# Kernel optimization log

Measured on AMD Instinct MI355X. Metric: run time of the kernel, lower is better.

Reference implementation:

```python
import jax, jax.numpy as jnp
import numpy as np


def setup_inputs() -> dict:
    key = jax.random.key(0)
    k1, k2, k3 = jax.random.split(key, 3)
    B, N, D = 4, 256, 128
    s = jax.random.normal(k1, (B, N, D), dtype=jnp.float32)
    W1 = jax.random.normal(k2, (3 * D, 2 * D), dtype=jnp.float32) * 0.02
    b1 = jnp.zeros((2 * D,), dtype=jnp.float32)
    W2 = jax.random.normal(k3, (2 * D, 1), dtype=jnp.float32) * 0.02
    b2 = jnp.zeros((1,), dtype=jnp.float32)
    return {"s": s, "W1": W1, "b1": b1, "W2": W2, "b2": b2, "K": 8}


def reference(s, W1, b1, W2, b2, K):
    B, N, D = s.shape
    si = jnp.broadcast_to(s[:, :, None, :], (B, N, N, D))
    sj = jnp.broadcast_to(s[:, None, :, :], (B, N, N, D))
    pair = jnp.concatenate([si, sj, si * sj], axis=-1)  # [B,N,N,3D]
    h = jax.nn.relu(pair @ W1 + b1)                      # [B,N,N,2D]
    scores = (h @ W2 + b2)[..., 0]                       # [B,N,N]
    k = min(int(K), N)
    _, idx = jax.lax.top_k(scores, k)                    # [B,N,K]
    # scatter ones at topk indices (indices are distinct per row)
    gate = jnp.sum(jax.nn.one_hot(idx, N, dtype=jnp.float32), axis=-2)  # [B,N,N]
    w = gate / jnp.clip(jnp.sum(gate, axis=-1, keepdims=True), 1.0)
    ctx = jnp.einsum('bij,bjd->bid', w, s)               # [B,N,D]
    return ctx, gate, w
```

## Files before the change

### kernel.cpp

```cpp
#include <hip/hip_runtime.h>
#include <hip/hip_bf16.h>
#include <math.h>

#define B_ 4
#define N_ 256
#define D_ 128
#define H_ 256
#define K_ 8

typedef __attribute__((ext_vector_type(8))) short short8;
typedef __attribute__((ext_vector_type(4))) float f32x4;

__device__ __forceinline__ unsigned short f2bf(float x) {
    union { __hip_bfloat16 h; unsigned short s; } u;
    u.h = __float2bfloat16(x);
    return u.s;
}
__device__ __forceinline__ float bf2f(unsigned short b) {
    unsigned v = ((unsigned)b) << 16;
    return __builtin_bit_cast(float, v);
}
__device__ __forceinline__ unsigned pk2(float x, float y) {
    union { __hip_bfloat162 h; unsigned u; } c;
    c.h = __float22bfloat162_rn(float2{x, y});
    return c.u;
}
__device__ __forceinline__ void gld_lds16(const float* g, float* l) {
    __builtin_amdgcn_global_load_lds(
        (const __attribute__((address_space(1))) void*)g,
        (__attribute__((address_space(3))) void*)l, 16, 0, 0);
}

__global__ __launch_bounds__(256) void pre_kernel(
    const float* __restrict__ s, const float* __restrict__ W1,
    const float* __restrict__ b1,
    float* __restrict__ avec, float* __restrict__ bvec,
    unsigned short* __restrict__ Wt)
{
    int blk = blockIdx.x;
    int t = threadIdx.x;
    if (blk < 512) {
        int bi0 = blk * 2;
        __shared__ float s2[2][D_];
        {
            int r = t >> 7, d = t & 127;
            s2[r][d] = s[(size_t)(bi0 + r) * D_ + d];
        }
        __syncthreads();
        float aA0 = b1[t], aA1 = aA0, aB0 = 0.f, aB1 = 0.f;
        const float* W1a = W1 + t;
        const float* W1b = W1 + (size_t)D_ * H_ + t;
        #pragma unroll 8
        for (int d = 0; d < D_; ++d) {
            float wa = W1a[(size_t)d * H_];
            float wb = W1b[(size_t)d * H_];
            float s0 = s2[0][d], s1 = s2[1][d];
            aA0 = fmaf(s0, wa, aA0);
            aA1 = fmaf(s1, wa, aA1);
            aB0 = fmaf(s0, wb, aB0);
            aB1 = fmaf(s1, wb, aB1);
        }
        avec[(size_t)bi0 * H_ + t]       = aA0;
        avec[(size_t)(bi0 + 1) * H_ + t] = aA1;
        bvec[(size_t)bi0 * H_ + t]       = aB0;
        bvec[(size_t)(bi0 + 1) * H_ + t] = aB1;
    } else {
        int e = (blk - 512) * 256 + t;
        int h = e >> 7, d = e & 127;
        Wt[e] = f2bf(W1[(size_t)(2 * D_ + d) * H_ + h]);
    }
}

__global__ __launch_bounds__(512, 2) void approx_scores(
    const float* __restrict__ s, const unsigned short* __restrict__ Wt,
    const float* __restrict__ W2, const float* __restrict__ b2,
    const float* __restrict__ avec, const float* __restrict__ bvec,
    unsigned short* __restrict__ ascu)
{
    int blk = blockIdx.x;
    int b   = blk >> 7;
    int jtb = ((blk >> 4) & 7) * 32;
    int i0  = (blk & 15) * 16;
    int t = threadIdx.x;
    int lane = t & 63;
    int w = __builtin_amdgcn_readfirstlane(t >> 6);
    int l15 = lane & 15, quad = lane >> 4;

    __shared__ __align__(16) short Pl[2][32 * 128];
    __shared__ __align__(16) float si_all[16][D_];
    __shared__ float partial[2][8][32];

    const float* sB = s + (size_t)b * N_ * D_;

    {
        int ii = t >> 5, dq = t & 31;
        *(float4*)&si_all[ii][dq * 4] =
            *(const float4*)(sB + (size_t)(i0 + ii) * D_ + dq * 4);
    }

    short8 Wreg[2][4];
    #pragma unroll
    for (int mi = 0; mi < 2; ++mi)
        #pragma unroll
        for (int dk = 0; dk < 4; ++dk)
            Wreg[mi][dk] = *(const short8*)(
                Wt + (size_t)(w * 32 + mi * 16 + l15) * D_ + dk * 32 + quad * 8);
    float bvr[2][2][4];
    float w2r[2][4];
    #pragma unroll
    for (int mi = 0; mi < 2; ++mi) {
        int hq = w * 32 + mi * 16 + quad * 4;
        #pragma unroll
        for (int r = 0; r < 4; ++r)
            w2r[mi][r] = W2[hq + r];
        #pragma unroll
        for (int nj = 0; nj < 2; ++nj)
            #pragma unroll
            for (int r = 0; r < 4; ++r)
                bvr[mi][nj][r] = bvec[((size_t)(b * N_ + jtb + nj * 16 + l15)) * H_
                                      + hq + r];
    }
    float b2v = b2[0];
    __syncthreads();

    {
        int row = t >> 4, seg = t & 15;
        const float* sj = sB + (size_t)(jtb + row) * D_ + seg * 8;
        float4 a0 = ((const float4*)sj)[0], a1 = ((const float4*)sj)[1];
        const float* si = &si_all[0][seg * 8];
        float4 s0 = ((const float4*)si)[0], s1 = ((const float4*)si)[1];
        uint4 v;
        v.x = pk2(a0.x * s0.x, a0.y * s0.y);
        v.y = pk2(a0.z * s0.z, a0.w * s0.w);
        v.z = pk2(a1.x * s1.x, a1.y * s1.y);
        v.w = pk2(a1.z * s1.z, a1.w * s1.w);
        int pc = seg ^ (row & 15);
        *(uint4*)&Pl[0][row * 128 + pc * 8] = v;
    }
    __syncthreads();

    #pragma unroll 1
    for (int i = 0; i < 16; ++i) {
        int cur = i & 1;
        if (w == 0 && lane < 32 && i > 0) {
            float sum = b2v;
            #pragma unroll
            for (int ww = 0; ww < 8; ++ww) sum += partial[(i - 1) & 1][ww][lane];
            ascu[(size_t)(b * N_ + i0 + i - 1) * N_ + jtb + lane] = f2bf(sum);
        }
        float avc[2][4];
        #pragma unroll
        for (int mi = 0; mi < 2; ++mi) {
            int hq = w * 32 + mi * 16 + quad * 4;
            #pragma unroll
            for (int r = 0; r < 4; ++r)
                avc[mi][r] = avec[(size_t)(b * N_ + i0 + i) * H_ + hq + r];
        }
        f32x4 acc[2][2];
        #pragma unroll
        for (int mi = 0; mi < 2; ++mi)
            #pragma unroll
            for (int nj = 0; nj < 2; ++nj)
                acc[mi][nj] = (f32x4){0.f, 0.f, 0.f, 0.f};
        #pragma unroll
        for (int dk = 0; dk < 4; ++dk) {
            short8 Pf[2];
            #pragma unroll
            for (int nj = 0; nj < 2; ++nj) {
                int pcc = (dk * 4 + quad) ^ l15;
                Pf[nj] = *(const short8*)&Pl[cur][(nj * 16 + l15) * 128 + pcc * 8];
            }
            #pragma unroll
            for (int nj = 0; nj < 2; ++nj)
                #pragma unroll
                for (int mi = 0; mi < 2; ++mi)
                    acc[mi][nj] = __builtin_amdgcn_mfma_f32_16x16x32_bf16(
                        Wreg[mi][dk], Pf[nj], acc[mi][nj], 0, 0, 0);
        }
        if (i < 15) {
            int row = t >> 4, seg = t & 15;
            const float* sj = sB + (size_t)(jtb + row) * D_ + seg * 8;
            float4 a0 = ((const float4*)sj)[0], a1 = ((const float4*)sj)[1];
            const float* si = &si_all[i + 1][seg * 8];
            float4 s0 = ((const float4*)si)[0], s1 = ((const float4*)si)[1];
            uint4 v;
            v.x = pk2(a0.x * s0.x, a0.y * s0.y);
            v.y = pk2(a0.z * s0.z, a0.w * s0.w);
            v.z = pk2(a1.x * s1.x, a1.y * s1.y);
            v.w = pk2(a1.z * s1.z, a1.w * s1.w);
            int pc = seg ^ (row & 15);
            *(uint4*)&Pl[cur ^ 1][row * 128 + pc * 8] = v;
        }
        float rs[2];
        rs[0] = 0.f; rs[1] = 0.f;
        #pragma unroll
        for (int mi = 0; mi < 2; ++mi)
            #pragma unroll
            for (int nj = 0; nj < 2; ++nj)
                #pragma unroll
                for (int r = 0; r < 4; ++r) {
                    float z = acc[mi][nj][r] + avc[mi][r] + bvr[mi][nj][r];
                    rs[nj] = fmaf(fmaxf(z, 0.f), w2r[mi][r], rs[nj]);
                }
        #pragma unroll
        for (int nj = 0; nj < 2; ++nj) {
            rs[nj] += __shfl_xor(rs[nj], 16);
            rs[nj] += __shfl_xor(rs[nj], 32);
        }
        if (lane < 32) {
            float v = (quad == 0) ? rs[0] : rs[1];
            partial[cur][w][lane] = v;
        }
        __syncthreads();
    }
    if (w == 0 && lane < 32) {
        float sum = b2v;
        #pragma unroll
        for (int ww = 0; ww < 8; ++ww) sum += partial[15 & 1][ww][lane];
        ascu[(size_t)(b * N_ + i0 + 15) * N_ + jtb + lane] = f2bf(sum);
    }
}

#define DC8 8
__global__ __launch_bounds__(256) void finalize_kernel(
    const float* __restrict__ s, const float* __restrict__ W1,
    const float* __restrict__ W2, const float* __restrict__ b2,
    const float* __restrict__ avec, const float* __restrict__ bvec,
    const unsigned short* __restrict__ ascu,
    float* __restrict__ ctx, float* __restrict__ gate, float* __restrict__ w)
{
    int bi0 = blockIdx.x * 2;
    int b = bi0 >> 8;
    int t = threadIdx.x;

    __shared__ float asc[2][N_];
    __shared__ int cand[2][16];
    __shared__ __align__(16) float Pt[D_ * 32];
    __shared__ __align__(16) float Wl[2][DC8 * H_];
    __shared__ float part[2][16][33];
    __shared__ float rsc[2][16];
    __shared__ int sel8[2][8];

    for (int e = t; e < 512; e += 256) {
        int r = e >> 8, jj = e & 255;
        asc[r][jj] = bf2f(ascu[(size_t)(bi0 + r) * N_ + jj]);
    }
    __syncthreads();

    {
        int r = t >> 7, lj = t & 127;
        float my[2]; int rk[2];
        #pragma unroll
        for (int m = 0; m < 2; ++m) { my[m] = asc[r][m * 128 + lj]; rk[m] = 0; }
        #pragma unroll 4
        for (int j2 = 0; j2 < N_; ++j2) {
            float o = asc[r][j2];
            #pragma unroll
            for (int m = 0; m < 2; ++m) {
                int jm = m * 128 + lj;
                rk[m] += (o > my[m]) || (o == my[m] && j2 < jm);
            }
        }
        #pragma unroll
        for (int m = 0; m < 2; ++m)
            if (rk[m] < 16) cand[r][rk[m]] = m * 128 + lj;
    }
    __syncthreads();

    const float* Wc = W1 + (size_t)2 * D_ * H_;

    #pragma unroll
    for (int k = 0; k < 2; ++k) {
        int slot = t + 256 * k;
        gld_lds16(Wc + slot * 4, &Wl[0][slot * 4]);
    }

    for (int e = t; e < 1024; e += 256) {
        int rr = e >> 9, c = e & 15, dq = (e >> 4) & 31;
        int j = cand[rr][c];
        float4 sj = *(const float4*)(s + ((size_t)(b * N_ + j)) * D_ + dq * 4);
        float4 si = *(const float4*)(s + ((size_t)(bi0 + rr)) * D_ + dq * 4);
        int base = (dq * 4) * 32 + rr * 16 + c;
        Pt[base + 0 * 32] = si.x * sj.x;
        Pt[base + 1 * 32] = si.y * sj.y;
        Pt[base + 2 * 32] = si.z * sj.z;
        Pt[base + 3 * 32] = si.w * sj.w;
    }

    int cg = t & 3, rr = (t >> 2) & 1;
    int hg = t >> 3;
    int h0 = hg * 8;
    float acc[4][8];
    {
        const float* av = avec + (size_t)(bi0 + rr) * H_ + h0;
        float4 av40 = *(const float4*)(av);
        float4 av41 = *(const float4*)(av + 4);
        #pragma unroll
        for (int cc = 0; cc < 4; ++cc) {
            int j = cand[rr][cg * 4 + cc];
            const float* bv = bvec + ((size_t)(b * N_ + j)) * H_ + h0;
            float4 b40 = *(const float4*)(bv);
            float4 b41 = *(const float4*)(bv + 4);
            acc[cc][0] = av40.x + b40.x;
            acc[cc][1] = av40.y + b40.y;
            acc[cc][2] = av40.z + b40.z;
            acc[cc][3] = av40.w + b40.w;
            acc[cc][4] = av41.x + b41.x;
            acc[cc][5] = av41.y + b41.y;
            acc[cc][6] = av41.z + b41.z;
            acc[cc][7] = av41.w + b41.w;
        }
    }
    __syncthreads();

    int pvoff = rr * 16 + cg * 4;
    #pragma unroll 1
    for (int ch = 0; ch < 16; ++ch) {
        int cur = ch & 1;
        if (ch < 15) {
            const float* src = Wc + (size_t)(ch + 1) * DC8 * H_;
            #pragma unroll
            for (int k = 0; k < 2; ++k) {
                int slot = t + 256 * k;
                gld_lds16(src + slot * 4, &Wl[cur ^ 1][slot * 4]);
            }
        }
        int d0 = ch * DC8;
        #pragma unroll
        for (int d = 0; d < DC8; ++d) {
            float4 pv = *(const float4*)&Pt[(d0 + d) * 32 + pvoff];
            float wv[8];
            *(float4*)&wv[0] = *(const float4*)&Wl[cur][d * H_ + h0];
            *(float4*)&wv[4] = *(const float4*)&Wl[cur][d * H_ + h0 + 4];
            #pragma unroll
            for (int m = 0; m < 8; ++m) {
                acc[0][m] = fmaf(pv.x, wv[m], acc[0][m]);
                acc[1][m] = fmaf(pv.y, wv[m], acc[1][m]);
                acc[2][m] = fmaf(pv.z, wv[m], acc[2][m]);
                acc[3][m] = fmaf(pv.w, wv[m], acc[3][m]);
            }
        }
        __syncthreads();
    }

    {
        float w2v[8];
        *(float4*)&w2v[0] = *(const float4*)(W2 + h0);
        *(float4*)&w2v[4] = *(const float4*)(W2 + h0 + 4);
        #pragma unroll
        for (int cc = 0; cc < 4; ++cc) {
            float sc = 0.f;
            #pragma unroll
            for (int m = 0; m < 8; ++m)
                sc = fmaf(fmaxf(acc[cc][m], 0.f), w2v[m], sc);
            part[rr][cg * 4 + cc][hg] = sc;
        }
    }
    __syncthreads();
    if (t < 32) {
        int r2 = t >> 4, c2 = t & 15;
        float sum = b2[0];
        #pragma unroll
        for (int m = 0; m < 32; ++m) sum += part[r2][c2][m];
        rsc[r2][c2] = sum;
    }
    __syncthreads();

    if (t < 32) {
        int r2 = t >> 4, c2 = t & 15;
        float my = rsc[r2][c2]; int myj = cand[r2][c2];
        int rank = 0;
        #pragma unroll
        for (int c3 = 0; c3 < 16; ++c3) {
            float o = rsc[r2][c3]; int oj = cand[r2][c3];
            rank += (o > my) || (o == my && oj < myj);
        }
        if (rank < 8) sel8[r2][rank] = myj;
    }
    __syncthreads();

    for (int e = t; e < 512; e += 256) {
        int r2 = e >> 8, jj = e & 255;
        float gv = 0.f;
        #pragma unroll
        for (int m = 0; m < 8; ++m)
            gv = (jj == sel8[r2][m]) ? 1.f : gv;
        gate[(size_t)(bi0 + r2) * N_ + jj] = gv;
        w[(size_t)(bi0 + r2) * N_ + jj]    = gv * 0.125f;
    }
    {
        int r2 = t >> 7, d = t & 127;
        float a = 0.f;
        #pragma unroll
        for (int m = 0; m < 8; ++m)
            a += s[((size_t)(b * N_ + sel8[r2][m])) * D_ + d];
        ctx[(size_t)(bi0 + r2) * D_ + d] = a * 0.125f;
    }
}

extern "C" void kernel_launch(void* const* d_in, const int* in_sizes, int n_in,
                              void* d_out, int out_size, void* d_ws, size_t ws_size,
                              hipStream_t stream)
{
    const float* s  = (const float*)d_in[0];
    const float* W1 = (const float*)d_in[1];
    const float* b1 = (const float*)d_in[2];
    const float* W2 = (const float*)d_in[3];
    const float* b2 = (const float*)d_in[4];

    float* avec = (float*)d_ws;
    float* bvec = avec + (size_t)B_ * N_ * H_;
    unsigned short* ascu = (unsigned short*)(bvec + (size_t)B_ * N_ * H_);
    unsigned short* Wtu  = ascu + (size_t)B_ * N_ * N_;

    float* ctx  = (float*)d_out;
    float* gate = ctx + (size_t)B_ * N_ * D_;
    float* wout = gate + (size_t)B_ * N_ * N_;

    pre_kernel<<<640, 256, 0, stream>>>(s, W1, b1, avec, bvec, Wtu);
    approx_scores<<<512, 512, 0, stream>>>(s, Wtu, W2, b2, avec, bvec, ascu);
    finalize_kernel<<<B_ * N_ / 2, 256, 0, stream>>>(s, W1, W2, b2, avec, bvec, ascu,
                                                     ctx, gate, wout);
}
```

Before: 130.0 us.

## Fuse approximate scoring and exact rescoring finalize into one kernel

After: 155.8 us. 19.9% more time.

```diff
diff --git a/kernel.cpp b/kernel.cpp
--- a/kernel.cpp
+++ b/kernel.cpp
@@ -7,6 +7,7 @@
 #define D_ 128
 #define H_ 256
 #define K_ 8
+#define DC8 8
 
 typedef __attribute__((ext_vector_type(8))) short short8;
 typedef __attribute__((ext_vector_type(4))) float f32x4;
@@ -15,10 +16,6 @@
     union { __hip_bfloat16 h; unsigned short s; } u;
     u.h = __float2bfloat16(x);
     return u.s;
-}
-__device__ __forceinline__ float bf2f(unsigned short b) {
-    unsigned v = ((unsigned)b) << 16;
-    return __builtin_bit_cast(float, v);
 }
 __device__ __forceinline__ unsigned pk2(float x, float y) {
     union { __hip_bfloat162 h; unsigned u; } c;
@@ -71,31 +68,46 @@
     }
 }
 
-__global__ __launch_bounds__(512, 2) void approx_scores(
+__global__ __launch_bounds__(512, 2) void mega_kernel(
     const float* __restrict__ s, const unsigned short* __restrict__ Wt,
-    const float* __restrict__ W2, const float* __restrict__ b2,
+    const float* __restrict__ W1, const float* __restrict__ W2,
+    const float* __restrict__ b2,
     const float* __restrict__ avec, const float* __restrict__ bvec,
-    unsigned short* __restrict__ ascu)
+    float* __restrict__ ctx, float* __restrict__ gate,
+    float* __restrict__ wout)
 {
     int blk = blockIdx.x;
+    int bi0 = blk * 2;
     int b   = blk >> 7;
-    int jtb = ((blk >> 4) & 7) * 32;
-    int i0  = (blk & 15) * 16;
     int t = threadIdx.x;
     int lane = t & 63;
-    int w = __builtin_amdgcn_readfirstlane(t >> 6);
+    int wq = __builtin_amdgcn_readfirstlane(t >> 6);
     int l15 = lane & 15, quad = lane >> 4;
-
-    __shared__ __align__(16) short Pl[2][32 * 128];
-    __shared__ __align__(16) float si_all[16][D_];
-    __shared__ float partial[2][8][32];
+    int prow = t >> 4, pseg = t & 15;
+
+    __shared__ float asc[2][N_];
+    union U {
+        struct {
+            short Pl[2][32 * 128];
+            float si2[2][D_];
+            float partial[2][8][32];
+        } p;
+        struct {
+            float Pt[D_ * 32];
+            float Wl[2][DC8 * H_];
+            float partW[8][2][16];
+            float rsc[2][16];
+            int   cand[2][16];
+            int   sel8[2][8];
+        } c;
+    };
+    __shared__ __align__(16) U sm;
 
     const float* sB = s + (size_t)b * N_ * D_;
 
-    {
-        int ii = t >> 5, dq = t & 31;
-        *(float4*)&si_all[ii][dq * 4] =
-            *(const float4*)(sB + (size_t)(i0 + ii) * D_ + dq * 4);
+    if (t < 256) {
+        int r = t >> 7, d = t & 127;
+        sm.p.si2[r][d] = s[(size_t)(bi0 + r) * D_ + d];
     }
 
     short8 Wreg[2][4];
@@ -104,71 +116,72 @@
         #pragma unroll
         for (int dk = 0; dk < 4; ++dk)
             Wreg[mi][dk] = *(const short8*)(
-                Wt + (size_t)(w * 32 + mi * 16 + l15) * D_ + dk * 32 + quad * 8);
-    float bvr[2][2][4];
+                Wt + (size_t)(wq * 32 + mi * 16 + l15) * D_ + dk * 32 + quad * 8);
     float w2r[2][4];
+    float4 av4[2][2];
     #pragma unroll
     for (int mi = 0; mi < 2; ++mi) {
-        int hq = w * 32 + mi * 16 + quad * 4;
+        int hq = wq * 32 + mi * 16 + quad * 4;
         #pragma unroll
         for (int r = 0; r < 4; ++r)
             w2r[mi][r] = W2[hq + r];
         #pragma unroll
-        for (int nj = 0; nj < 2; ++nj)
-            #pragma unroll
-            for (int r = 0; r < 4; ++r)
-                bvr[mi][nj][r] = bvec[((size_t)(b * N_ + jtb + nj * 16 + l15)) * H_
-                                      + hq + r];
+        for (int ir = 0; ir < 2; ++ir)
+            av4[ir][mi] = *(const float4*)&avec[(size_t)(bi0 + ir) * H_ + hq];
     }
     float b2v = b2[0];
     __syncthreads();
 
     {
-        int row = t >> 4, seg = t & 15;
-        const float* sj = sB + (size_t)(jtb + row) * D_ + seg * 8;
+        const float* sj = sB + (size_t)(0 * 32 + prow) * D_ + pseg * 8;
         float4 a0 = ((const float4*)sj)[0], a1 = ((const float4*)sj)[1];
-        const float* si = &si_all[0][seg * 8];
+        const float* si = &sm.p.si2[0][pseg * 8];
         float4 s0 = ((const float4*)si)[0], s1 = ((const float4*)si)[1];
         uint4 v;
         v.x = pk2(a0.x * s0.x, a0.y * s0.y);
         v.y = pk2(a0.z * s0.z, a0.w * s0.w);
         v.z = pk2(a1.x * s1.x, a1.y * s1.y);
         v.w = pk2(a1.z * s1.z, a1.w * s1.w);
-        int pc = seg ^ (row & 15);
-        *(uint4*)&Pl[0][row * 128 + pc * 8] = v;
+        int pc = pseg ^ (prow & 15);
+        *(uint4*)&sm.p.Pl[0][prow * 128 + pc * 8] = v;
     }
     __syncthreads();
 
     #pragma unroll 1
-    for (int i = 0; i < 16; ++i) {
-        int cur = i & 1;
-        if (w == 0 && lane < 32 && i > 0) {
+    for (int r = 0; r < 16; ++r) {
+        int cur = r & 1;
+        int ir = r >> 3, jt = r & 7;
+        if (wq == 0 && lane < 32 && r > 0) {
+            int pr = r - 1;
             float sum = b2v;
             #pragma unroll
-            for (int ww = 0; ww < 8; ++ww) sum += partial[(i - 1) & 1][ww][lane];
-            ascu[(size_t)(b * N_ + i0 + i - 1) * N_ + jtb + lane] = f2bf(sum);
-        }
-        float avc[2][4];
-        #pragma unroll
-        for (int mi = 0; mi < 2; ++mi) {
-            int hq = w * 32 + mi * 16 + quad * 4;
-            #pragma unroll
-            for (int r = 0; r < 4; ++r)
-                avc[mi][r] = avec[(size_t)(b * N_ + i0 + i) * H_ + hq + r];
-        }
+            for (int ww = 0; ww < 8; ++ww)
+                sum += sm.p.partial[pr & 1][ww][lane];
+            asc[pr >> 3][(pr & 7) * 32 + lane] = sum;
+        }
+        float4 bv4[2][2];
+        #pragma unroll
+        for (int mi = 0; mi < 2; ++mi)
+            #pragma unroll
+            for (int nj = 0; nj < 2; ++nj)
+                bv4[mi][nj] = *(const float4*)&bvec[
+                    ((size_t)(b * N_ + jt * 32 + nj * 16 + l15)) * H_
+                    + wq * 32 + mi * 16 + quad * 4];
         f32x4 acc[2][2];
         #pragma unroll
         for (int mi = 0; mi < 2; ++mi)
             #pragma unroll
             for (int nj = 0; nj < 2; ++nj)
-                acc[mi][nj] = (f32x4){0.f, 0.f, 0.f, 0.f};
+                #pragma unroll
+                for (int rx = 0; rx < 4; ++rx)
+                    acc[mi][nj][rx] = av4[ir][mi][rx];
         #pragma unroll
         for (int dk = 0; dk < 4; ++dk) {
             short8 Pf[2];
             #pragma unroll
             for (int nj = 0; nj < 2; ++nj) {
                 int pcc = (dk * 4 + quad) ^ l15;
-                Pf[nj] = *(const short8*)&Pl[cur][(nj * 16 + l15) * 128 + pcc * 8];
+                Pf[nj] = *(const short8*)&sm.p.Pl[cur][(nj * 16 + l15) * 128 + pcc * 8];
             }
             #pragma unroll
             for (int nj = 0; nj < 2; ++nj)
@@ -177,19 +190,20 @@
                     acc[mi][nj] = __builtin_amdgcn_mfma_f32_16x16x32_bf16(
                         Wreg[mi][dk], Pf[nj], acc[mi][nj], 0, 0, 0);
         }
-        if (i < 15) {
-            int row = t >> 4, seg = t & 15;
-            const float* sj = sB + (size_t)(jtb + row) * D_ + seg * 8;
+        if (r < 15) {
+            int nr = r + 1;
+            int ir2 = nr >> 3, jt2 = nr & 7;
+            const float* sj = sB + (size_t)(jt2 * 32 + prow) * D_ + pseg * 8;
             float4 a0 = ((const float4*)sj)[0], a1 = ((const float4*)sj)[1];
-            const float* si = &si_all[i + 1][seg * 8];
+            const float* si = &sm.p.si2[ir2][pseg * 8];
             float4 s0 = ((const float4*)si)[0], s1 = ((const float4*)si)[1];
             uint4 v;
             v.x = pk2(a0.x * s0.x, a0.y * s0.y);
             v.y = pk2(a0.z * s0.z, a0.w * s0.w);
             v.z = pk2(a1.x * s1.x, a1.y * s1.y);
             v.w = pk2(a1.z * s1.z, a1.w * s1.w);
-            int pc = seg ^ (row & 15);
-            *(uint4*)&Pl[cur ^ 1][row * 128 + pc * 8] = v;
+            int pc = pseg ^ (prow & 15);
+            *(uint4*)&sm.p.Pl[cur ^ 1][prow * 128 + pc * 8] = v;
         }
         float rs[2];
         rs[0] = 0.f; rs[1] = 0.f;
@@ -198,9 +212,9 @@
             #pragma unroll
             for (int nj = 0; nj < 2; ++nj)
                 #pragma unroll
-                for (int r = 0; r < 4; ++r) {
-                    float z = acc[mi][nj][r] + avc[mi][r] + bvr[mi][nj][r];
-                    rs[nj] = fmaf(fmaxf(z, 0.f), w2r[mi][r], rs[nj]);
+                for (int rx = 0; rx < 4; ++rx) {
+                    float z = acc[mi][nj][rx] + bv4[mi][nj][rx];
+                    rs[nj] = fmaf(fmaxf(z, 0.f), w2r[mi][rx], rs[nj]);
                 }
         #pragma unroll
         for (int nj = 0; nj < 2; ++nj) {
@@ -209,135 +223,90 @@
         }
         if (lane < 32) {
             float v = (quad == 0) ? rs[0] : rs[1];
-            partial[cur][w][lane] = v;
+            sm.p.partial[cur][wq][lane] = v;
         }
         __syncthreads();
     }
-    if (w == 0 && lane < 32) {
+    if (wq == 0 && lane < 32) {
         float sum = b2v;
         #pragma unroll
-        for (int ww = 0; ww < 8; ++ww) sum += partial[15 & 1][ww][lane];
-        ascu[(size_t)(b * N_ + i0 + 15) * N_ + jtb + lane] = f2bf(sum);
-    }
-}
-
-#define DC8 8
-__global__ __launch_bounds__(256) void finalize_kernel(
-    const float* __restrict__ s, const float* __restrict__ W1,
-    const float* __restrict__ W2, const float* __restrict__ b2,
-    const float* __restrict__ avec, const float* __restrict__ bvec,
-    const unsigned short* __restrict__ ascu,
-    float* __restrict__ ctx, float* __restrict__ gate, float* __restrict__ w)
-{
-    int bi0 = blockIdx.x * 2;
-    int b = bi0 >> 8;
-    int t = threadIdx.x;
-
-    __shared__ float asc[2][N_];
-    __shared__ int cand[2][16];
-    __shared__ __align__(16) float Pt[D_ * 32];
-    __shared__ __align__(16) float Wl[2][DC8 * H_];
-    __shared__ float part[2][16][33];
-    __shared__ float rsc[2][16];
-    __shared__ int sel8[2][8];
-
-    for (int e = t; e < 512; e += 256) {
-        int r = e >> 8, jj = e & 255;
-        asc[r][jj] = bf2f(ascu[(size_t)(bi0 + r) * N_ + jj]);
-    }
-    __syncthreads();
-
-    {
-        int r = t >> 7, lj = t & 127;
-        float my[2]; int rk[2];
-        #pragma unroll
-        for (int m = 0; m < 2; ++m) { my[m] = asc[r][m * 128 + lj]; rk[m] = 0; }
+        for (int ww = 0; ww < 8; ++ww)
+            sum += sm.p.partial[1][ww][lane];
+        asc[1][7 * 32 + lane] = sum;
+    }
+    __syncthreads();
+
+    {
+        int r2 = t >> 8, lj = t & 255;
+        float my = asc[r2][lj]; int rk = 0;
         #pragma unroll 4
         for (int j2 = 0; j2 < N_; ++j2) {
-            float o = asc[r][j2];
-            #pragma unroll
-            for (int m = 0; m < 2; ++m) {
-                int jm = m * 128 + lj;
-                rk[m] += (o > my[m]) || (o == my[m] && j2 < jm);
-            }
-        }
-        #pragma unroll
-        for (int m = 0; m < 2; ++m)
-            if (rk[m] < 16) cand[r][rk[m]] = m * 128 + lj;
+            float o = asc[r2][j2];
+            rk += (o > my) || (o == my && j2 < lj);
+        }
+        if (rk < 16) sm.c.cand[r2][rk] = lj;
     }
     __syncthreads();
 
     const float* Wc = W1 + (size_t)2 * D_ * H_;
 
-    #pragma unroll
-    for (int k = 0; k < 2; ++k) {
-        int slot = t + 256 * k;
-        gld_lds16(Wc + slot * 4, &Wl[0][slot * 4]);
-    }
-
-    for (int e = t; e < 1024; e += 256) {
+    gld_lds16(Wc + t * 4, &sm.c.Wl[0][0] + t * 4);
+
+    for (int e = t; e < 1024; e += 512) {
         int rr = e >> 9, c = e & 15, dq = (e >> 4) & 31;
-        int j = cand[rr][c];
+        int j = sm.c.cand[rr][c];
         float4 sj = *(const float4*)(s + ((size_t)(b * N_ + j)) * D_ + dq * 4);
         float4 si = *(const float4*)(s + ((size_t)(bi0 + rr)) * D_ + dq * 4);
         int base = (dq * 4) * 32 + rr * 16 + c;
-        Pt[base + 0 * 32] = si.x * sj.x;
-        Pt[base + 1 * 32] = si.y * sj.y;
-        Pt[base + 2 * 32] = si.z * sj.z;
-        Pt[base + 3 * 32] = si.w * sj.w;
-    }
-
-    int cg = t & 3, rr = (t >> 2) & 1;
-    int hg = t >> 3;
+        sm.c.Pt[base + 0 * 32] = si.x * sj.x;
+        sm.c.Pt[base + 1 * 32] = si.y * sj.y;
+        sm.c.Pt[base + 2 * 32] = si.z * sj.z;
+        sm.c.Pt[base + 3 * 32] = si.w * sj.w;
+    }
+
+    int cg2 = t & 7, rr = (t >> 3) & 1, hg = t >> 4;
     int h0 = hg * 8;
-    float acc[4][8];
+    float facc[2][8];
     {
         const float* av = avec + (size_t)(bi0 + rr) * H_ + h0;
         float4 av40 = *(const float4*)(av);
         float4 av41 = *(const float4*)(av + 4);
         #pragma unroll
-        for (int cc = 0; cc < 4; ++cc) {
-            int j = cand[rr][cg * 4 + cc];
+        for (int cc = 0; cc < 2; ++cc) {
+            int j = sm.c.cand[rr][cg2 * 2 + cc];
             const float* bv = bvec + ((size_t)(b * N_ + j)) * H_ + h0;
             float4 b40 = *(const float4*)(bv);
             float4 b41 = *(const float4*)(bv + 4);
-            acc[cc][0] = av40.x + b40.x;
-            acc[cc][1] = av40.y + b40.y;
-            acc[cc][2] = av40.z + b40.z;
-            acc[cc][3] = av40.w + b40.w;
-            acc[cc][4] = av41.x + b41.x;
-            acc[cc][5] = av41.y + b41.y;
-            acc[cc][6] = av41.z + b41.z;
-            acc[cc][7] = av41.w + b41.w;
-        }
-    }
-    __syncthreads();
-
-    int pvoff = rr * 16 + cg * 4;
+            facc[cc][0] = av40.x + b40.x;
+            facc[cc][1] = av40.y + b40.y;
+            facc[cc][2] = av40.z + b40.z;
+            facc[cc][3] = av40.w + b40.w;
+            facc[cc][4] = av41.x + b41.x;
+            facc[cc][5] = av41.y + b41.y;
+            facc[cc][6] = av41.z + b41.z;
+            facc[cc][7] = av41.w + b41.w;
+        }
+    }
+    __syncthreads();
+
+    int pvoff = rr * 16 + cg2 * 2;
     #pragma unroll 1
     for (int ch = 0; ch < 16; ++ch) {
         int cur = ch & 1;
-        if (ch < 15) {
-            const float* src = Wc + (size_t)(ch + 1) * DC8 * H_;
-            #pragma unroll
-            for (int k = 0; k < 2; ++k) {
-                int slot = t + 256 * k;
-                gld_lds16(src + slot * 4, &Wl[cur ^ 1][slot * 4]);
-            }
-        }
+        if (ch < 15)
+            gld_lds16(Wc + (size_t)(ch + 1) * DC8 * H_ + t * 4,
+                      &sm.c.Wl[cur ^ 1][0] + t * 4);
         int d0 = ch * DC8;
         #pragma unroll
         for (int d = 0; d < DC8; ++d) {
-            float4 pv = *(const float4*)&Pt[(d0 + d) * 32 + pvoff];
+            float2 pv = *(const float2*)&sm.c.Pt[(d0 + d) * 32 + pvoff];
             float wv[8];
-            *(float4*)&wv[0] = *(const float4*)&Wl[cur][d * H_ + h0];
-            *(float4*)&wv[4] = *(const float4*)&Wl[cur][d * H_ + h0 + 4];
+            *(float4*)&wv[0] = *(const float4*)&sm.c.Wl[cur][d * H_ + h0];
+            *(float4*)&wv[4] = *(const float4*)&sm.c.Wl[cur][d * H_ + h0 + 4];
             #pragma unroll
             for (int m = 0; m < 8; ++m) {
-                acc[0][m] = fmaf(pv.x, wv[m], acc[0][m]);
-                acc[1][m] = fmaf(pv.y, wv[m], acc[1][m]);
-                acc[2][m] = fmaf(pv.z, wv[m], acc[2][m]);
-                acc[3][m] = fmaf(pv.w, wv[m], acc[3][m]);
+                facc[0][m] = fmaf(pv.x, wv[m], facc[0][m]);
+                facc[1][m] = fmaf(pv.y, wv[m], facc[1][m]);
             }
         }
         __syncthreads();
@@ -347,53 +316,56 @@
         float w2v[8];
         *(float4*)&w2v[0] = *(const float4*)(W2 + h0);
         *(float4*)&w2v[4] = *(const float4*)(W2 + h0 + 4);
-        #pragma unroll
-        for (int cc = 0; cc < 4; ++cc) {
+        int wv_id = t >> 6;
+        #pragma unroll
+        for (int cc = 0; cc < 2; ++cc) {
             float sc = 0.f;
             #pragma unroll
             for (int m = 0; m < 8; ++m)
-                sc = fmaf(fmaxf(acc[cc][m], 0.f), w2v[m], sc);
-            part[rr][cg * 4 + cc][hg] = sc;
+                sc = fmaf(fmaxf(facc[cc][m], 0.f), w2v[m], sc);
+            sc += __shfl_xor(sc, 16);
+            sc += __shfl_xor(sc, 32);
+            if (lane < 16) sm.c.partW[wv_id][rr][cg2 * 2 + cc] = sc;
         }
     }
     __syncthreads();
     if (t < 32) {
         int r2 = t >> 4, c2 = t & 15;
-        float sum = b2[0];
-        #pragma unroll
-        for (int m = 0; m < 32; ++m) sum += part[r2][c2][m];
-        rsc[r2][c2] = sum;
+        float sum = b2v;
+        #pragma unroll
+        for (int wv2 = 0; wv2 < 8; ++wv2) sum += sm.c.partW[wv2][r2][c2];
+        sm.c.rsc[r2][c2] = sum;
     }
     __syncthreads();
 
     if (t < 32) {
         int r2 = t >> 4, c2 = t & 15;
-        float my = rsc[r2][c2]; int myj = cand[r2][c2];
+        float my = sm.c.rsc[r2][c2]; int myj = sm.c.cand[r2][c2];
         int rank = 0;
         #pragma unroll
         for (int c3 = 0; c3 < 16; ++c3) {
-            float o = rsc[r2][c3]; int oj = cand[r2][c3];
+            float o = sm.c.rsc[r2][c3]; int oj = sm.c.cand[r2][c3];
             rank += (o > my) || (o == my && oj < myj);
         }
-        if (rank < 8) sel8[r2][rank] = myj;
-    }
-    __syncthreads();
-
-    for (int e = t; e < 512; e += 256) {
-        int r2 = e >> 8, jj = e & 255;
+        if (rank < 8) sm.c.sel8[r2][rank] = myj;
+    }
+    __syncthreads();
+
+    {
+        int r2 = t >> 8, jj = t & 255;
         float gv = 0.f;
         #pragma unroll
         for (int m = 0; m < 8; ++m)
-            gv = (jj == sel8[r2][m]) ? 1.f : gv;
+            gv = (jj == sm.c.sel8[r2][m]) ? 1.f : gv;
         gate[(size_t)(bi0 + r2) * N_ + jj] = gv;
-        w[(size_t)(bi0 + r2) * N_ + jj]    = gv * 0.125f;
-    }
-    {
+        wout[(size_t)(bi0 + r2) * N_ + jj] = gv * 0.125f;
+    }
+    if (t < 256) {
         int r2 = t >> 7, d = t & 127;
         float a = 0.f;
         #pragma unroll
         for (int m = 0; m < 8; ++m)
-            a += s[((size_t)(b * N_ + sel8[r2][m])) * D_ + d];
+            a += s[((size_t)(b * N_ + sm.c.sel8[r2][m])) * D_ + d];
         ctx[(size_t)(bi0 + r2) * D_ + d] = a * 0.125f;
     }
 }
@@ -410,15 +382,13 @@
 
     float* avec = (float*)d_ws;
     float* bvec = avec + (size_t)B_ * N_ * H_;
-    unsigned short* ascu = (unsigned short*)(bvec + (size_t)B_ * N_ * H_);
-    unsigned short* Wtu  = ascu + (size_t)B_ * N_ * N_;
+    unsigned short* Wtu = (unsigned short*)(bvec + (size_t)B_ * N_ * H_);
 
     float* ctx  = (float*)d_out;
     float* gate = ctx + (size_t)B_ * N_ * D_;
     float* wout = gate + (size_t)B_ * N_ * N_;
 
     pre_kernel<<<640, 256, 0, stream>>>(s, W1, b1, avec, bvec, Wtu);
-    approx_scores<<<512, 512, 0, stream>>>(s, Wtu, W2, b2, avec, bvec, ascu);
-    finalize_kernel<<<B_ * N_ / 2, 256, 0, stream>>>(s, W1, W2, b2, avec, bvec, ascu,
-                                                     ctx, gate, wout);
-}
+    mega_kernel<<<512, 512, 0, stream>>>(s, Wtu, W1, W2, b2, avec, bvec,
+                                         ctx, gate, wout);
+}
```
